# Performance work log

Hardware: AMD Instinct MI355X
Metric: run time of the kernel (lower is better)

The kernel has to match this reference:

```python
import jax, jax.numpy as jnp
import numpy as np

ALPHA = 0.2          # leaky relu negative slope (init arg alpha)
NEG_BIG = -9.0e15    # matches -9000000000000000.0 mask value in source


def setup_inputs() -> dict:
    key = jax.random.key(0)
    k1, k2, k3, k4, k5 = jax.random.split(key, 5)
    N, Fin, Fout = 8192, 512, 64
    input = jax.random.normal(k1, (N, Fin), dtype=jnp.float32)
    adj = jax.random.randint(k2, (N, N), 0, 2, dtype=jnp.int32)
    W = jax.random.normal(k3, (Fin, Fout), dtype=jnp.float32) * (1.0 / np.sqrt(Fout))
    a = jax.random.normal(k4, (2 * Fout, 1), dtype=jnp.float32) * (1.0 / np.sqrt(Fout))
    bias = jax.random.normal(k5, (Fout,), dtype=jnp.float32) * (1.0 / np.sqrt(Fout))
    return {"input": input, "adj": adj, "W": W, "a": a, "bias": bias}


def reference(input, adj, W, a, bias):
    Fout = W.shape[1]
    z = input @ W                                  # [N, Fout]
    # ConcatAll + matmul with a is equivalent to a1^T z_i + a2^T z_j
    a1 = a[:Fout, 0]                               # [Fout]
    a2 = a[Fout:, 0]                               # [Fout]
    s1 = z @ a1                                    # [N] score for source node i
    s2 = z @ a2                                    # [N] score for target node j
    e = jax.nn.leaky_relu(s1[:, None] + s2[None, :], negative_slope=ALPHA)  # [N, N]
    eij = jnp.where(adj > 0, e, NEG_BIG)
    attention = jax.nn.softmax(eij, axis=1)        # torch F.softmax default dim=1 for 2D
    output = attention @ z                         # [N, Fout]
    return output + bias
```

## Files before the change

### kernel.cpp

```cpp
#include <hip/hip_runtime.h>

typedef float    f32x4  __attribute__((ext_vector_type(4)));
typedef __bf16   bf16x8 __attribute__((ext_vector_type(8)));
typedef unsigned short u16;
typedef unsigned int   u32;
typedef unsigned long long u64;
typedef unsigned short u16x8 __attribute__((ext_vector_type(8)));
typedef int      i32x4  __attribute__((ext_vector_type(4)));

#define NN   8192
#define FIN  512
#define FOUT 64
#define LOG2E 1.4426950408889634f

#if __has_builtin(__builtin_amdgcn_exp2f)
#define EXP2F(x) __builtin_amdgcn_exp2f(x)
#else
#define EXP2F(x) exp2f(x)
#endif

__device__ __forceinline__ u16 f2bf(float f) {
    unsigned int u = __float_as_uint(f);
    u += 0x7FFFu + ((u >> 16) & 1u);
    return (u16)(u >> 16);
}
__device__ __forceinline__ float bf2f(u16 b) {
    return __uint_as_float(((unsigned int)b) << 16);
}
__device__ __forceinline__ u32 spread4(u32 x) {
    x = (x | (x << 12)) & 0x000F000Fu;
    x = (x | (x <<  6)) & 0x03030303u;
    x = (x | (x <<  3)) & 0x11111111u;
    return x;
}

__global__ __launch_bounds__(256) void k_wt(const float* __restrict__ W,
                                            u16* __restrict__ wt_hi,
                                            u16* __restrict__ wt_lo) {
    int t = blockIdx.x * 256 + threadIdx.x;
    int k = t >> 6, c = t & 63;
    float w = W[t];
    u16 h = f2bf(w);
    wt_hi[c * FIN + k] = h;
    wt_lo[c * FIN + k] = f2bf(w - bf2f(h));
}

__global__ __launch_bounds__(128) void k_zgemm(
        const float* __restrict__ in, const u16* __restrict__ wt_hi,
        const u16* __restrict__ wt_lo, const float* __restrict__ a,
        u16* __restrict__ zt, float* __restrict__ s1p, float* __restrict__ s2p)
{
    __shared__ f32x4 xch[4][64];
    const int wv = threadIdx.x >> 6;
    const int l  = threadIdx.x & 63;
    const int lr = l & 15, lk = l >> 4;
    const int row_base = blockIdx.x * 16;

    f32x4 acc[4] = {};
    const float* inrow = in + (size_t)(row_base + lr) * FIN;

    for (int ks = wv * 8; ks < wv * 8 + 8; ++ks) {
        const int k0 = ks * 32 + lk * 8;
        const f32x4 v0 = *(const f32x4*)(inrow + k0);
        const f32x4 v1 = *(const f32x4*)(inrow + k0 + 4);
        u16x8 hv, lv;
#pragma unroll
        for (int i = 0; i < 4; ++i) {
            u16 h = f2bf(v0[i]); hv[i] = h; lv[i] = f2bf(v0[i] - bf2f(h));
        }
#pragma unroll
        for (int i = 0; i < 4; ++i) {
            u16 h = f2bf(v1[i]); hv[4 + i] = h; lv[4 + i] = f2bf(v1[i] - bf2f(h));
        }
        const bf16x8 ahi = __builtin_bit_cast(bf16x8, hv);
        const bf16x8 alo = __builtin_bit_cast(bf16x8, lv);
#pragma unroll
        for (int nt = 0; nt < 4; ++nt) {
            const int wrow = nt * 16 + lr;
            const bf16x8 bh = __builtin_bit_cast(bf16x8, *(const u16x8*)(wt_hi + (size_t)wrow * FIN + k0));
            const bf16x8 bl = __builtin_bit_cast(bf16x8, *(const u16x8*)(wt_lo + (size_t)wrow * FIN + k0));
            acc[nt] = __builtin_amdgcn_mfma_f32_16x16x32_bf16(ahi, bh, acc[nt], 0, 0, 0);
            acc[nt] = __builtin_amdgcn_mfma_f32_16x16x32_bf16(alo, bh, acc[nt], 0, 0, 0);
            acc[nt] = __builtin_amdgcn_mfma_f32_16x16x32_bf16(ahi, bl, acc[nt], 0, 0, 0);
        }
    }

    if (wv == 1) {
#pragma unroll
        for (int nt = 0; nt < 4; ++nt) xch[nt][l] = acc[nt];
    }
    __syncthreads();
    if (wv == 1) return;
#pragma unroll
    for (int nt = 0; nt < 4; ++nt) acc[nt] += xch[nt][l];

#pragma unroll
    for (int nt = 0; nt < 4; ++nt)
#pragma unroll
        for (int r = 0; r < 4; ++r) {
            const int j = row_base + lk * 4 + r;
            const int c = nt * 16 + lr;
            zt[(size_t)(j >> 3) * 512 + c * 8 + (j & 7)] = f2bf(acc[nt][r]);
        }

    float a1c[4], a2c[4];
#pragma unroll
    for (int nt = 0; nt < 4; ++nt) {
        a1c[nt] = a[nt * 16 + lr];
        a2c[nt] = a[64 + nt * 16 + lr];
    }
#pragma unroll
    for (int r = 0; r < 4; ++r) {
        float s1 = 0.f, s2 = 0.f;
#pragma unroll
        for (int nt = 0; nt < 4; ++nt) {
            s1 += acc[nt][r] * a1c[nt];
            s2 += acc[nt][r] * a2c[nt];
        }
#pragma unroll
        for (int m = 1; m <= 8; m <<= 1) {
            s1 += __shfl_xor(s1, m, 64);
            s2 += __shfl_xor(s2, m, 64);
        }
        if (lr == 0) {
            s1p[row_base + lk * 4 + r] = s1 * LOG2E;
            s2p[row_base + lk * 4 + r] = s2 * LOG2E;
        }
    }
}

#define LOADZ(Z0, Z1, Z2, Z3, jn) do {                                        \
    const u16* _zb = zq + (size_t)(((jn) + jb) >> 3) * 512;                   \
    Z0 = *(const u16x8*)(_zb +   0);                                          \
    Z1 = *(const u16x8*)(_zb + 128);                                          \
    Z2 = *(const u16x8*)(_zb + 256);                                          \
    Z3 = *(const u16x8*)(_zb + 384); } while (0)

#define LOADS2T(T0, T1, jn) do {                                              \
    T0 = *(const f32x4*)(s2r + (jn));                                         \
    T1 = *(const f32x4*)(s2r + (jn) + 4); } while (0)

#define LBLK(V0, V1, V2, V3, TT) do {                                         \
    V0 = *(const i32x4*)(aB + 0 * NN + (TT) * 256);                           \
    V1 = *(const i32x4*)(aB + 1 * NN + (TT) * 256);                           \
    V2 = *(const i32x4*)(aB + 2 * NN + (TT) * 256);                           \
    V3 = *(const i32x4*)(aB + 3 * NN + (TT) * 256); } while (0)

#define SROW(V, RI, MB) do {                                                  \
    const u64 _B0 = __ballot(V[0] != 0);                                      \
    const u64 _B1 = __ballot(V[1] != 0);                                      \
    const u64 _B2 = __ballot(V[2] != 0);                                      \
    const u64 _B3 = __ballot(V[3] != 0);                                      \
    if (l < 8) {                                                              \
        const u32 _w = spread4((u32)(_B0 >> (l * 8)) & 0xFFu)                 \
                     | (spread4((u32)(_B1 >> (l * 8)) & 0xFFu) << 1)          \
                     | (spread4((u32)(_B2 >> (l * 8)) & 0xFFu) << 2)          \
                     | (spread4((u32)(_B3 >> (l * 8)) & 0xFFu) << 3);         \
        maskt[MB][wv * 4 + (RI)][l] = _w;                                     \
    } } while (0)

#define SBLK(V0, V1, V2, V3, TT) do {                                         \
    const int _mb = (TT) & 1;                                                 \
    SROW(V0, 0, _mb); SROW(V1, 1, _mb);                                       \
    SROW(V2, 2, _mb); SROW(V3, 3, _mb); } while (0)

#define LOADBT(BB0, BB1, TT) do {                                             \
    BB0 = maskt[(TT) & 1][lr][wv];                                            \
    BB1 = maskt[(TT) & 1][lr + 16][wv]; } while (0)

#define WAVEBAR() do {                                                        \
    asm volatile("s_waitcnt lgkmcnt(0)" ::: "memory");                        \
    __builtin_amdgcn_s_barrier();                                             \
    asm volatile("" ::: "memory"); } while (0)

#define PHA(WF, BW, S0, S1, S1R, DD) do {                                     \
    const u32 bsh = (BW) >> (lk * 8);                                         \
    _Pragma("unroll")                                                         \
    for (int i = 0; i < 4; ++i) {                                             \
        const float y = (S1R) + S0[i];                                        \
        float w = EXP2F(fmaxf(y, 0.2f * y));                                  \
        w = ((bsh >> i) & 1u) ? w : 0.0f;                                     \
        const __bf16 wb = (__bf16)w;                                          \
        WF[i] = wb; DD += (float)wb; }                                        \
    _Pragma("unroll")                                                         \
    for (int i = 0; i < 4; ++i) {                                             \
        const float y = (S1R) + S1[i];                                        \
        float w = EXP2F(fmaxf(y, 0.2f * y));                                  \
        w = ((bsh >> (4 + i)) & 1u) ? w : 0.0f;                               \
        const __bf16 wb = (__bf16)w;                                          \
        WF[4 + i] = wb; DD += (float)wb; } } while (0)

#define MFMA8(WF0, WF1, Z0, Z1, Z2, Z3) do {                                  \
    acc00 = __builtin_amdgcn_mfma_f32_16x16x32_bf16(WF0, __builtin_bit_cast(bf16x8, Z0), acc00, 0, 0, 0); \
    acc01 = __builtin_amdgcn_mfma_f32_16x16x32_bf16(WF0, __builtin_bit_cast(bf16x8, Z1), acc01, 0, 0, 0); \
    acc02 = __builtin_amdgcn_mfma_f32_16x16x32_bf16(WF0, __builtin_bit_cast(bf16x8, Z2), acc02, 0, 0, 0); \
    acc03 = __builtin_amdgcn_mfma_f32_16x16x32_bf16(WF0, __builtin_bit_cast(bf16x8, Z3), acc03, 0, 0, 0); \
    acc10 = __builtin_amdgcn_mfma_f32_16x16x32_bf16(WF1, __builtin_bit_cast(bf16x8, Z0), acc10, 0, 0, 0); \
    acc11 = __builtin_amdgcn_mfma_f32_16x16x32_bf16(WF1, __builtin_bit_cast(bf16x8, Z1), acc11, 0, 0, 0); \
    acc12 = __builtin_amdgcn_mfma_f32_16x16x32_bf16(WF1, __builtin_bit_cast(bf16x8, Z2), acc12, 0, 0, 0); \
    acc13 = __builtin_amdgcn_mfma_f32_16x16x32_bf16(WF1, __builtin_bit_cast(bf16x8, Z3), acc13, 0, 0, 0); } while (0)

#define BODYJ(CZ0,CZ1,CZ2,CZ3, NZ0,NZ1,NZ2,NZ3, SV0,SV1,SV2,SV3,              \
              LV0,LV1,LV2,LV3, SC0,SC1,SN0,SN1, JT, F_S, F_L, F_NXT) do {     \
    WAVEBAR();                                                                \
    u32 B0t, B1t;                                                             \
    LOADBT(B0t, B1t, JT);                                                     \
    if (F_S) SBLK(SV0, SV1, SV2, SV3, (JT) + 1);                              \
    if (F_L) LBLK(LV0, LV1, LV2, LV3, (JT) + 2);                              \
    if (F_NXT) { LOADZ(NZ0, NZ1, NZ2, NZ3, (JT) * 256 + 256);                 \
                 LOADS2T(SN0, SN1, (JT) * 256 + 256); }                       \
    bf16x8 wf0, wf1;                                                          \
    PHA(wf0, B0t, SC0, SC1, s1r0, d0);                                        \
    PHA(wf1, B1t, SC0, SC1, s1r1, d1);                                        \
    MFMA8(wf0, wf1, CZ0, CZ1, CZ2, CZ3); } while (0)

__global__ __launch_bounds__(512, 2) void k_attn(
        const int* __restrict__ adj, const u16* __restrict__ zt,
        const float* __restrict__ s1p, const float* __restrict__ s2p,
        const float* __restrict__ bias, float* __restrict__ out)
{
    __shared__ float apart[8][32][64];
    __shared__ float dpart[8][4][32];
    __shared__ u32   maskt[2][32][9];

    const int t  = threadIdx.x;
    const int wv = t >> 6, l = t & 63;
    const int lr = l & 15, lk = l >> 4;
    const int row0 = blockIdx.x * 32;
    const int jb = wv * 32 + lk * 8;

    const float s1r0 = s1p[row0 + lr];
    const float s1r1 = s1p[row0 + 16 + lr];
    const float* s2r  = s2p + jb;
    const u16*   zq   = zt + lr * 8;
    const int*   aB   = adj + (size_t)(row0 + wv * 4) * NN + l * 4;

    f32x4 acc00{}, acc01{}, acc02{}, acc03{};
    f32x4 acc10{}, acc11{}, acc12{}, acc13{};
    float d0 = 0.f, d1 = 0.f;

    u16x8 zU0, zU1, zU2, zU3, zV0, zV1, zV2, zV3;
    i32x4 qA0, qA1, qA2, qA3, qB0, qB1, qB2, qB3;
    f32x4 sA0, sA1, sB0, sB1;

    LOADZ(zU0, zU1, zU2, zU3, 0);
    LOADS2T(sA0, sA1, 0);
    LBLK(qA0, qA1, qA2, qA3, 0);
    LBLK(qB0, qB1, qB2, qB3, 1);
    SBLK(qA0, qA1, qA2, qA3, 0);

    for (int jt = 0; jt < 30; jt += 2) {
        BODYJ(zU0, zU1, zU2, zU3, zV0, zV1, zV2, zV3,
              qB0, qB1, qB2, qB3, qA0, qA1, qA2, qA3,
              sA0, sA1, sB0, sB1, jt, 1, 1, 1);
        BODYJ(zV0, zV1, zV2, zV3, zU0, zU1, zU2, zU3,
              qA0, qA1, qA2, qA3, qB0, qB1, qB2, qB3,
              sB0, sB1, sA0, sA1, jt + 1, 1, 1, 1);
    }
    BODYJ(zU0, zU1, zU2, zU3, zV0, zV1, zV2, zV3,
          qB0, qB1, qB2, qB3, qA0, qA1, qA2, qA3,
          sA0, sA1, sB0, sB1, 30, 1, 0, 1);
    BODYJ(zV0, zV1, zV2, zV3, zU0, zU1, zU2, zU3,
          qA0, qA1, qA2, qA3, qB0, qB1, qB2, qB3,
          sB0, sB1, sA0, sA1, 31, 0, 0, 0);

    dpart[wv][lk][lr]      = d0;
    dpart[wv][lk][16 + lr] = d1;
#pragma unroll
    for (int r = 0; r < 4; ++r) {
        apart[wv][lk * 4 + r][ 0 + lr] = acc00[r];
        apart[wv][lk * 4 + r][16 + lr] = acc01[r];
        apart[wv][lk * 4 + r][32 + lr] = acc02[r];
        apart[wv][lk * 4 + r][48 + lr] = acc03[r];
        apart[wv][16 + lk * 4 + r][ 0 + lr] = acc10[r];
        apart[wv][16 + lk * 4 + r][16 + lr] = acc11[r];
        apart[wv][16 + lk * 4 + r][32 + lr] = acc12[r];
        apart[wv][16 + lk * 4 + r][48 + lr] = acc13[r];
    }
    __syncthreads();

    {
        const int r  = t >> 4;
        const int c0 = (t & 15) * 4;
        float den = 0.f;
#pragma unroll
        for (int q = 0; q < 32; ++q)
            den += dpart[q >> 2][q & 3][r];
        f32x4 val = {};
#pragma unroll
        for (int q = 0; q < 8; ++q)
            val += *(const f32x4*)&apart[q][r][c0];
        const f32x4 bv = *(const f32x4*)(bias + c0);
        const f32x4 o = val * (1.0f / den) + bv;
        *(f32x4*)(out + (size_t)(row0 + r) * FOUT + c0) = o;
    }
}

extern "C" void kernel_launch(void* const* d_in, const int* in_sizes, int n_in,
                              void* d_out, int out_size, void* d_ws, size_t ws_size,
                              hipStream_t stream) {
    const float* input = (const float*)d_in[0];
    const int*   adj   = (const int*)d_in[1];
    const float* W     = (const float*)d_in[2];
    const float* a     = (const float*)d_in[3];
    const float* bias  = (const float*)d_in[4];
    float* out = (float*)d_out;

    char* ws = (char*)d_ws;
    u16*   wt_hi = (u16*)ws;   ws += FIN * FOUT * sizeof(u16);
    u16*   wt_lo = (u16*)ws;   ws += FIN * FOUT * sizeof(u16);
    float* s1p   = (float*)ws; ws += NN * sizeof(float);
    float* s2p   = (float*)ws; ws += NN * sizeof(float);
    u16*   zt    = (u16*)ws;   ws += (size_t)NN * FOUT * sizeof(u16);

    k_wt   <<<dim3(128), dim3(256), 0, stream>>>(W, wt_hi, wt_lo);
    k_zgemm<<<dim3(512), dim3(128), 0, stream>>>(input, wt_hi, wt_lo, a, zt, s1p, s2p);
    k_attn <<<dim3(256), dim3(512), 0, stream>>>(adj, zt, s1p, s2p, bias, out);
}
```

Before: 81.24 us.

## Split attention columns into two halves with a combine kernel, drop z double-buffer

The attention kernel now splits each 32-row block's 8192 columns into two halves, launching 512 blocks instead of 256. Each block writes unnormalized partial sums and denominators to workspace, and a new combine kernel adds the halves, normalizes and adds bias. The z and s2 register double-buffering is removed in favour of loading in the same iteration, and launch bounds ask for 4 blocks per CU. This targets fuller occupancy of the 256-CU GPU, since 256 blocks filled it poorly. In exchange it adds an extra kernel launch, partial-result traffic through global memory, and exposed z-load latency.

```diff
diff --git a/kernel.cpp b/kernel.cpp
--- a/kernel.cpp
+++ b/kernel.cpp
@@ -129,16 +129,16 @@
     }
 }
 
-#define LOADZ(Z0, Z1, Z2, Z3, jn) do {                                        \
+#define LOADZ(jn) do {                                                        \
     const u16* _zb = zq + (size_t)(((jn) + jb) >> 3) * 512;                   \
-    Z0 = *(const u16x8*)(_zb +   0);                                          \
-    Z1 = *(const u16x8*)(_zb + 128);                                          \
-    Z2 = *(const u16x8*)(_zb + 256);                                          \
-    Z3 = *(const u16x8*)(_zb + 384); } while (0)
-
-#define LOADS2T(T0, T1, jn) do {                                              \
-    T0 = *(const f32x4*)(s2r + (jn));                                         \
-    T1 = *(const f32x4*)(s2r + (jn) + 4); } while (0)
+    zU0 = *(const u16x8*)(_zb +   0);                                         \
+    zU1 = *(const u16x8*)(_zb + 128);                                         \
+    zU2 = *(const u16x8*)(_zb + 256);                                         \
+    zU3 = *(const u16x8*)(_zb + 384); } while (0)
+
+#define LOADS2T(jn) do {                                                      \
+    sA0 = *(const f32x4*)(s2r + (jn));                                        \
+    sA1 = *(const f32x4*)(s2r + (jn) + 4); } while (0)
 
 #define LBLK(V0, V1, V2, V3, TT) do {                                         \
     V0 = *(const i32x4*)(aB + 0 * NN + (TT) * 256);                           \
@@ -190,34 +190,33 @@
         const __bf16 wb = (__bf16)w;                                          \
         WF[4 + i] = wb; DD += (float)wb; } } while (0)
 
-#define MFMA8(WF0, WF1, Z0, Z1, Z2, Z3) do {                                  \
-    acc00 = __builtin_amdgcn_mfma_f32_16x16x32_bf16(WF0, __builtin_bit_cast(bf16x8, Z0), acc00, 0, 0, 0); \
-    acc01 = __builtin_amdgcn_mfma_f32_16x16x32_bf16(WF0, __builtin_bit_cast(bf16x8, Z1), acc01, 0, 0, 0); \
-    acc02 = __builtin_amdgcn_mfma_f32_16x16x32_bf16(WF0, __builtin_bit_cast(bf16x8, Z2), acc02, 0, 0, 0); \
-    acc03 = __builtin_amdgcn_mfma_f32_16x16x32_bf16(WF0, __builtin_bit_cast(bf16x8, Z3), acc03, 0, 0, 0); \
-    acc10 = __builtin_amdgcn_mfma_f32_16x16x32_bf16(WF1, __builtin_bit_cast(bf16x8, Z0), acc10, 0, 0, 0); \
-    acc11 = __builtin_amdgcn_mfma_f32_16x16x32_bf16(WF1, __builtin_bit_cast(bf16x8, Z1), acc11, 0, 0, 0); \
-    acc12 = __builtin_amdgcn_mfma_f32_16x16x32_bf16(WF1, __builtin_bit_cast(bf16x8, Z2), acc12, 0, 0, 0); \
-    acc13 = __builtin_amdgcn_mfma_f32_16x16x32_bf16(WF1, __builtin_bit_cast(bf16x8, Z3), acc13, 0, 0, 0); } while (0)
-
-#define BODYJ(CZ0,CZ1,CZ2,CZ3, NZ0,NZ1,NZ2,NZ3, SV0,SV1,SV2,SV3,              \
-              LV0,LV1,LV2,LV3, SC0,SC1,SN0,SN1, JT, F_S, F_L, F_NXT) do {     \
+#define MFMA8(WF0, WF1) do {                                                  \
+    acc00 = __builtin_amdgcn_mfma_f32_16x16x32_bf16(WF0, __builtin_bit_cast(bf16x8, zU0), acc00, 0, 0, 0); \
+    acc01 = __builtin_amdgcn_mfma_f32_16x16x32_bf16(WF0, __builtin_bit_cast(bf16x8, zU1), acc01, 0, 0, 0); \
+    acc02 = __builtin_amdgcn_mfma_f32_16x16x32_bf16(WF0, __builtin_bit_cast(bf16x8, zU2), acc02, 0, 0, 0); \
+    acc03 = __builtin_amdgcn_mfma_f32_16x16x32_bf16(WF0, __builtin_bit_cast(bf16x8, zU3), acc03, 0, 0, 0); \
+    acc10 = __builtin_amdgcn_mfma_f32_16x16x32_bf16(WF1, __builtin_bit_cast(bf16x8, zU0), acc10, 0, 0, 0); \
+    acc11 = __builtin_amdgcn_mfma_f32_16x16x32_bf16(WF1, __builtin_bit_cast(bf16x8, zU1), acc11, 0, 0, 0); \
+    acc12 = __builtin_amdgcn_mfma_f32_16x16x32_bf16(WF1, __builtin_bit_cast(bf16x8, zU2), acc12, 0, 0, 0); \
+    acc13 = __builtin_amdgcn_mfma_f32_16x16x32_bf16(WF1, __builtin_bit_cast(bf16x8, zU3), acc13, 0, 0, 0); } while (0)
+
+#define BODYJS(SV0, SV1, SV2, SV3, LV0, LV1, LV2, LV3, JT, F_S, F_L) do {     \
     WAVEBAR();                                                                \
     u32 B0t, B1t;                                                             \
     LOADBT(B0t, B1t, JT);                                                     \
+    LOADZ((JT) * 256);                                                        \
+    LOADS2T((JT) * 256);                                                      \
     if (F_S) SBLK(SV0, SV1, SV2, SV3, (JT) + 1);                              \
     if (F_L) LBLK(LV0, LV1, LV2, LV3, (JT) + 2);                              \
-    if (F_NXT) { LOADZ(NZ0, NZ1, NZ2, NZ3, (JT) * 256 + 256);                 \
-                 LOADS2T(SN0, SN1, (JT) * 256 + 256); }                       \
     bf16x8 wf0, wf1;                                                          \
-    PHA(wf0, B0t, SC0, SC1, s1r0, d0);                                        \
-    PHA(wf1, B1t, SC0, SC1, s1r1, d1);                                        \
-    MFMA8(wf0, wf1, CZ0, CZ1, CZ2, CZ3); } while (0)
-
-__global__ __launch_bounds__(512, 2) void k_attn(
+    PHA(wf0, B0t, sA0, sA1, s1r0, d0);                                        \
+    PHA(wf1, B1t, sA0, sA1, s1r1, d1);                                        \
+    MFMA8(wf0, wf1); } while (0)
+
+__global__ __launch_bounds__(512, 4) void k_attn(
         const int* __restrict__ adj, const u16* __restrict__ zt,
         const float* __restrict__ s1p, const float* __restrict__ s2p,
-        const float* __restrict__ bias, float* __restrict__ out)
+        float* __restrict__ part, float* __restrict__ den)
 {
     __shared__ float apart[8][32][64];
     __shared__ float dpart[8][4][32];
@@ -226,43 +225,34 @@
     const int t  = threadIdx.x;
     const int wv = t >> 6, l = t & 63;
     const int lr = l & 15, lk = l >> 4;
-    const int row0 = blockIdx.x * 32;
+    const int half = blockIdx.x & 1;
+    const int row0 = (blockIdx.x >> 1) * 32;
     const int jb = wv * 32 + lk * 8;
 
     const float s1r0 = s1p[row0 + lr];
     const float s1r1 = s1p[row0 + 16 + lr];
-    const float* s2r  = s2p + jb;
-    const u16*   zq   = zt + lr * 8;
-    const int*   aB   = adj + (size_t)(row0 + wv * 4) * NN + l * 4;
+    const float* s2r = s2p + half * 4096 + jb;
+    const u16*   zq  = zt + (size_t)half * 262144 + lr * 8;
+    const int*   aB  = adj + (size_t)(row0 + wv * 4) * NN + half * 4096 + l * 4;
 
     f32x4 acc00{}, acc01{}, acc02{}, acc03{};
     f32x4 acc10{}, acc11{}, acc12{}, acc13{};
     float d0 = 0.f, d1 = 0.f;
 
-    u16x8 zU0, zU1, zU2, zU3, zV0, zV1, zV2, zV3;
+    u16x8 zU0, zU1, zU2, zU3;
     i32x4 qA0, qA1, qA2, qA3, qB0, qB1, qB2, qB3;
-    f32x4 sA0, sA1, sB0, sB1;
-
-    LOADZ(zU0, zU1, zU2, zU3, 0);
-    LOADS2T(sA0, sA1, 0);
+    f32x4 sA0, sA1;
+
     LBLK(qA0, qA1, qA2, qA3, 0);
     LBLK(qB0, qB1, qB2, qB3, 1);
     SBLK(qA0, qA1, qA2, qA3, 0);
 
-    for (int jt = 0; jt < 30; jt += 2) {
-        BODYJ(zU0, zU1, zU2, zU3, zV0, zV1, zV2, zV3,
-              qB0, qB1, qB2, qB3, qA0, qA1, qA2, qA3,
-              sA0, sA1, sB0, sB1, jt, 1, 1, 1);
-        BODYJ(zV0, zV1, zV2, zV3, zU0, zU1, zU2, zU3,
-              qA0, qA1, qA2, qA3, qB0, qB1, qB2, qB3,
-              sB0, sB1, sA0, sA1, jt + 1, 1, 1, 1);
-    }
-    BODYJ(zU0, zU1, zU2, zU3, zV0, zV1, zV2, zV3,
-          qB0, qB1, qB2, qB3, qA0, qA1, qA2, qA3,
-          sA0, sA1, sB0, sB1, 30, 1, 0, 1);
-    BODYJ(zV0, zV1, zV2, zV3, zU0, zU1, zU2, zU3,
-          qA0, qA1, qA2, qA3, qB0, qB1, qB2, qB3,
-          sB0, sB1, sA0, sA1, 31, 0, 0, 0);
+    for (int jt = 0; jt < 14; jt += 2) {
+        BODYJS(qB0, qB1, qB2, qB3, qA0, qA1, qA2, qA3, jt,     1, 1);
+        BODYJS(qA0, qA1, qA2, qA3, qB0, qB1, qB2, qB3, jt + 1, 1, 1);
+    }
+    BODYJS(qB0, qB1, qB2, qB3, qA0, qA1, qA2, qA3, 14, 1, 0);
+    BODYJS(qA0, qA1, qA2, qA3, qB0, qB1, qB2, qB3, 15, 0, 0);
 
     dpart[wv][lk][lr]      = d0;
     dpart[wv][lk][16 + lr] = d1;
@@ -282,18 +272,35 @@
     {
         const int r  = t >> 4;
         const int c0 = (t & 15) * 4;
-        float den = 0.f;
+        float dn = 0.f;
 #pragma unroll
         for (int q = 0; q < 32; ++q)
-            den += dpart[q >> 2][q & 3][r];
+            dn += dpart[q >> 2][q & 3][r];
         f32x4 val = {};
 #pragma unroll
         for (int q = 0; q < 8; ++q)
             val += *(const f32x4*)&apart[q][r][c0];
-        const f32x4 bv = *(const f32x4*)(bias + c0);
-        const f32x4 o = val * (1.0f / den) + bv;
-        *(f32x4*)(out + (size_t)(row0 + r) * FOUT + c0) = o;
-    }
+        float* ph = part + (size_t)half * NN * FOUT;
+        *(f32x4*)(ph + (size_t)(row0 + r) * FOUT + c0) = val;
+        if ((t & 15) == 0) den[half * NN + row0 + r] = dn;
+    }
+}
+
+__global__ __launch_bounds__(256) void k_comb(
+        const float* __restrict__ part, const float* __restrict__ den,
+        const float* __restrict__ bias, float* __restrict__ out)
+{
+    const int t = blockIdx.x * 256 + threadIdx.x;
+    const int e = t * 8;
+    const int r = e >> 6, c0 = e & 63;
+    const float* p0 = part;
+    const float* p1 = part + (size_t)NN * FOUT;
+    const f32x4 a0 = *(const f32x4*)(p0 + e), a1 = *(const f32x4*)(p0 + e + 4);
+    const f32x4 b0 = *(const f32x4*)(p1 + e), b1 = *(const f32x4*)(p1 + e + 4);
+    const float inv = 1.0f / (den[r] + den[NN + r]);
+    const f32x4 bv0 = *(const f32x4*)(bias + c0), bv1 = *(const f32x4*)(bias + c0 + 4);
+    *(f32x4*)(out + e)     = (a0 + b0) * inv + bv0;
+    *(f32x4*)(out + e + 4) = (a1 + b1) * inv + bv1;
 }
 
 extern "C" void kernel_launch(void* const* d_in, const int* in_sizes, int n_in,
@@ -312,8 +319,11 @@
     float* s1p   = (float*)ws; ws += NN * sizeof(float);
     float* s2p   = (float*)ws; ws += NN * sizeof(float);
     u16*   zt    = (u16*)ws;   ws += (size_t)NN * FOUT * sizeof(u16);
+    float* part  = (float*)ws; ws += (size_t)2 * NN * FOUT * sizeof(float);
+    float* den   = (float*)ws; ws += (size_t)2 * NN * sizeof(float);
 
     k_wt   <<<dim3(128), dim3(256), 0, stream>>>(W, wt_hi, wt_lo);
     k_zgemm<<<dim3(512), dim3(128), 0, stream>>>(input, wt_hi, wt_lo, a, zt, s1p, s2p);
-    k_attn <<<dim3(256), dim3(512), 0, stream>>>(adj, zt, s1p, s2p, bias, out);
-}
+    k_attn <<<dim3(512), dim3(512), 0, stream>>>(adj, zt, s1p, s2p, part, den);
+    k_comb <<<dim3(256), dim3(256), 0, stream>>>(part, den, bias, out);
+}
```

Result: slower. 84.19 us (+3.6%).
